# Performance work log

Measured on AMD Instinct MI355X. Metric: run time of the kernel, lower is better.

## Reference

```python
import jax, jax.numpy as jnp
import numpy as np

# dims (see shape_source): emb_dim=256, input_size=256 -> d_model=1024
B, L = 8, 1024
QUES = 4000
EMB = 256
DM = 1024          # input_size + 768
DI = 2048          # expand * d_model
N = 16             # d_state
DTR = 64           # dt_rank = ceil(d_model/16)
K = 4              # d_conv
EPS = 1e-12


def setup_inputs() -> dict:
    key = jax.random.key(0)
    ks = jax.random.split(key, 16)
    s = 0.02
    nrm = lambda k, sh: jax.random.normal(k, sh, dtype=jnp.float32) * s
    return {
        "x": jax.random.randint(ks[0], (B, L), 0, 2 * QUES + 1),
        "q_id": jax.random.randint(ks[1], (B, L), 0, QUES),
        "emb_table": nrm(ks[2], (2 * QUES + 1, EMB)),
        "ques_cont": nrm(ks[3], (QUES, 768)),
        "ln0_g": jnp.ones((DM,), jnp.float32),
        "ln0_b": jnp.zeros((DM,), jnp.float32),
        "in_proj_w": nrm(ks[4], (2 * DI, DM)),
        "conv_w": nrm(ks[5], (DI, K)),
        "conv_b": jnp.zeros((DI,), jnp.float32),
        "x_proj_w": nrm(ks[6], (DTR + 2 * N, DI)),
        "dt_proj_w": nrm(ks[7], (DI, DTR)),
        "dt_proj_b": nrm(ks[8], (DI,)),
        "A_log": jnp.log(jax.random.uniform(ks[9], (DI, N), jnp.float32, 1.0, 16.0)),
        "D_param": jnp.ones((DI,), jnp.float32),
        "out_proj_w": nrm(ks[10], (DM, DI)),
        "ln1_g": jnp.ones((DM,), jnp.float32),
        "ln1_b": jnp.zeros((DM,), jnp.float32),
        "fc_w": nrm(ks[11], (QUES, DM)),
        "fc_b": jnp.zeros((QUES,), jnp.float32),
    }


def _ln(x, g, b):
    m = x.mean(-1, keepdims=True)
    v = ((x - m) ** 2).mean(-1, keepdims=True)
    return (x - m) / jnp.sqrt(v + EPS) * g + b


def _mamba(xm, in_proj_w, conv_w, conv_b, x_proj_w, dt_proj_w, dt_proj_b,
           A_log, D_param, out_proj_w):
    # xm: [B, L, DM]
    u_r = xm @ in_proj_w.T                           # [B, L, 2*DI]
    u, r = jnp.split(u_r, 2, axis=-1)                # each [B, L, DI]
    Lq = u.shape[1]
    # causal depthwise conv1d (padding=K-1, truncated to L)
    u_pad = jnp.pad(u, ((0, 0), (K - 1, 0), (0, 0)))
    conv = sum(u_pad[:, k:k + Lq, :] * conv_w[:, k] for k in range(K)) + conv_b
    u = jax.nn.silu(conv)
    dbl = u @ x_proj_w.T                             # [B, L, DTR+2N]
    dt, Bm, Cm = dbl[..., :DTR], dbl[..., DTR:DTR + N], dbl[..., DTR + N:]
    delta = jax.nn.softplus(dt @ dt_proj_w.T + dt_proj_b)   # [B, L, DI]
    A = -jnp.exp(A_log)                              # [DI, N]

    def step(h, ins):
        d_t, b_t, c_t, u_t = ins                     # [B,DI],[B,N],[B,N],[B,DI]
        dA = jnp.exp(d_t[:, :, None] * A)            # [B, DI, N]
        h = dA * h + d_t[:, :, None] * b_t[:, None, :] * u_t[:, :, None]
        y_t = jnp.einsum('bdn,bn->bd', h, c_t)
        return h, y_t

    xs = (delta.transpose(1, 0, 2), Bm.transpose(1, 0, 2),
          Cm.transpose(1, 0, 2), u.transpose(1, 0, 2))
    h0 = jnp.zeros((u.shape[0], DI, N), u.dtype)
    _, ys = jax.lax.scan(step, h0, xs)               # ys: [L, B, DI]
    y = ys.transpose(1, 0, 2) + u * D_param
    y = y * jax.nn.silu(r)
    return y @ out_proj_w.T                          # [B, L, DM]


def reference(x, q_id, emb_table, ques_cont, ln0_g, ln0_b, in_proj_w, conv_w,
              conv_b, x_proj_w, dt_proj_w, dt_proj_b, A_log, D_param,
              out_proj_w, ln1_g, ln1_b, fc_w, fc_b):
    x_e = emb_table[x]                               # [B, L, 256]
    x_c = ques_cont[q_id]                            # [B, L, 768]
    item = _ln(jnp.concatenate([x_e, x_c], axis=-1), ln0_g, ln0_b)
    # source loop applies every layer to item_emb; only the last layer's
    # output is used, so compute exactly that one layer (num_layers=2 branch).
    h = _mamba(item, in_proj_w, conv_w, conv_b, x_proj_w, dt_proj_w,
               dt_proj_b, A_log, D_param, out_proj_w)
    out = _ln(h + item, ln1_g, ln1_b)
    return jax.nn.sigmoid(out @ fc_w.T + fc_b)       # [B, L, QUES]
```

## Files before the change

kernel.cpp:

```cpp
#include <hip/hip_runtime.h>
#include <cstdint>
#include <cstddef>

#define L_SEQ 1024
#define BATCH 8
#define DMODEL 1024
#define DINNER 2048
#define NSTATE 16
#define DTRANK 64
#define NQ 4000
#define NROWS (BATCH * L_SEQ)
#define CH 64
#define NCH (L_SEQ / CH)
#define XKN 96

typedef float f32x4 __attribute__((ext_vector_type(4)));
typedef __bf16 bf16x8 __attribute__((ext_vector_type(8)));

#define AS1 __attribute__((address_space(1)))
#define AS3 __attribute__((address_space(3)))

__device__ __forceinline__ unsigned short f2bf(float f) {
  union { float f; unsigned int u; } c; c.f = f;
  unsigned int u = c.u;
  unsigned int r = u + 0x7fffu + ((u >> 16) & 1u);
  return (unsigned short)(r >> 16);
}

__device__ __forceinline__ float sigmoidf_(float x) { return 1.f / (1.f + expf(-x)); }

__global__ void cast_bf16_k(const float* __restrict__ src, unsigned short* __restrict__ dst, int n) {
  int i = blockIdx.x * blockDim.x + threadIdx.x;
  if (i < n) dst[i] = f2bf(src[i]);
}

__device__ __forceinline__ float blk_sum(float v, float* s) {
  #pragma unroll
  for (int o = 32; o > 0; o >>= 1) v += __shfl_down(v, o, 64);
  int w = threadIdx.x >> 6;
  if ((threadIdx.x & 63) == 0) s[w] = v;
  __syncthreads();
  float r = s[0] + s[1] + s[2] + s[3];
  __syncthreads();
  return r;
}

__global__ __launch_bounds__(256) void embed_ln0_k(
    const int* __restrict__ x, const int* __restrict__ qid,
    const float* __restrict__ emb, const float* __restrict__ qc,
    const float* __restrict__ g, const float* __restrict__ bta,
    float* __restrict__ item, unsigned short* __restrict__ item_bf)
{
  __shared__ float sbuf[4];
  int i = blockIdx.x;
  int t = threadIdx.x;
  float4 v;
  if (t < 64) v = *(const float4*)&emb[(size_t)x[i] * 256 + t * 4];
  else        v = *(const float4*)&qc[(size_t)qid[i] * 768 + t * 4 - 256];
  float tot = blk_sum(v.x + v.y + v.z + v.w, sbuf);
  float mean = tot * (1.f / 1024.f);
  float dx = v.x - mean, dy = v.y - mean, dz = v.z - mean, dw = v.w - mean;
  float var = blk_sum(dx*dx + dy*dy + dz*dz + dw*dw, sbuf) * (1.f / 1024.f);
  float rstd = rsqrtf(var + 1e-12f);
  float vals[4] = {dx, dy, dz, dw};
  size_t rb = (size_t)i * 1024;
  #pragma unroll
  for (int j = 0; j < 4; j++) {
    int c = t * 4 + j;
    float o = vals[j] * rstd * g[c] + bta[c];
    item[rb + c] = o;
    item_bf[rb + c] = f2bf(o);
  }
}

template <int EPI>
__global__ __launch_bounds__(256) void gemm_bt_k(
    const unsigned short* __restrict__ A, const unsigned short* __restrict__ Bw,
    float* __restrict__ C, const float* __restrict__ bias,
    int M, int N, int K)
{
  __shared__ __align__(16) unsigned short As[128 * 64];
  __shared__ __align__(16) unsigned short Bs[128 * 64];
  const int tid = threadIdx.x;
  const int m0 = blockIdx.x * 128;
  const int n0 = blockIdx.y * 128;
  const int w = tid >> 6, lane = tid & 63;
  const int wrow = (w >> 1) * 64, wcol = (w & 1) * 64;
  const int quad = lane >> 4, lid = lane & 15;

  const int srow = lane >> 3;
  const int schunk = (lane & 7) ^ srow;

  const unsigned short* Abase = A + (size_t)(m0 + w * 8 + srow) * K + schunk * 8;
  const unsigned short* Bbase[4];
  #pragma unroll
  for (int i = 0; i < 4; i++) {
    int rB = n0 + w * 8 + i * 32 + srow;
    if (rB > N - 1) rB = N - 1;
    Bbase[i] = Bw + (size_t)rB * K + schunk * 8;
  }

  f32x4 acc[4][4] = {};

  for (int k0 = 0; k0 < K; k0 += 64) {
    #pragma unroll
    for (int i = 0; i < 4; i++) {
      int rA = w * 8 + i * 32;
      __builtin_amdgcn_global_load_lds(
          (const AS1 unsigned int*)(Abase + (size_t)i * 32 * K + k0),
          (AS3 unsigned int*)&As[rA * 64], 16, 0, 0);
      __builtin_amdgcn_global_load_lds(
          (const AS1 unsigned int*)(Bbase[i] + k0),
          (AS3 unsigned int*)&Bs[rA * 64], 16, 0, 0);
    }
    __syncthreads();
    #pragma unroll
    for (int kk = 0; kk < 64; kk += 32) {
      bf16x8 af[4], bfr[4];
      #pragma unroll
      for (int mi = 0; mi < 4; mi++) {
        int r = wrow + mi * 16 + lid;
        int slot = ((kk >> 3) + quad) ^ (lid & 7);
        af[mi] = *(const bf16x8*)&As[r * 64 + slot * 8];
      }
      #pragma unroll
      for (int ni = 0; ni < 4; ni++) {
        int r = wcol + ni * 16 + lid;
        int slot = ((kk >> 3) + quad) ^ (lid & 7);
        bfr[ni] = *(const bf16x8*)&Bs[r * 64 + slot * 8];
      }
      #pragma unroll
      for (int mi = 0; mi < 4; mi++)
        #pragma unroll
        for (int ni = 0; ni < 4; ni++)
          acc[mi][ni] = __builtin_amdgcn_mfma_f32_16x16x32_bf16(af[mi], bfr[ni], acc[mi][ni], 0, 0, 0);
    }
    __syncthreads();
  }

  #pragma unroll
  for (int mi = 0; mi < 4; mi++) {
    #pragma unroll
    for (int ni = 0; ni < 4; ni++) {
      int col = n0 + wcol + ni * 16 + lid;
      if (col >= N) continue;
      #pragma unroll
      for (int r = 0; r < 4; r++) {
        int row = m0 + wrow + mi * 16 + quad * 4 + r;
        float v = acc[mi][ni][r];
        if (EPI == 1) v = sigmoidf_(v + bias[col]);
        if (EPI == 2) { float xx = v + bias[col]; v = fmaxf(xx, 0.f) + log1pf(expf(-fabsf(xx))); }
        C[(size_t)row * N + col] = v;
      }
    }
  }
}

__global__ __launch_bounds__(256) void gemm_xk_k(
    const unsigned short* __restrict__ A, const unsigned short* __restrict__ Bw,
    float* __restrict__ slab, int M, int K, int KS)
{
  __shared__ __align__(16) unsigned short As[128 * 64];
  __shared__ __align__(16) unsigned short Bs[128 * 64];
  const int tid = threadIdx.x;
  const int m0 = blockIdx.x * 128;
  const int kslice = blockIdx.y;
  const int w = tid >> 6, lane = tid & 63;
  const int wrow = (w >> 1) * 64, wcol = (w & 1) * 64;
  const int quad = lane >> 4, lid = lane & 15;

  const int srow = lane >> 3;
  const int schunk = (lane & 7) ^ srow;

  const unsigned short* Abase = A + (size_t)(m0 + w * 8 + srow) * K + schunk * 8;
  const unsigned short* Bbase[4];
  #pragma unroll
  for (int i = 0; i < 4; i++) {
    int rB = w * 8 + i * 32 + srow;
    if (rB > XKN - 1) rB = XKN - 1;
    Bbase[i] = Bw + (size_t)rB * K + schunk * 8;
  }

  f32x4 acc[4][4] = {};
  const int kbeg = kslice * KS, kend = kbeg + KS;

  for (int k0 = kbeg; k0 < kend; k0 += 64) {
    #pragma unroll
    for (int i = 0; i < 4; i++) {
      int rA = w * 8 + i * 32;
      __builtin_amdgcn_global_load_lds(
          (const AS1 unsigned int*)(Abase + (size_t)i * 32 * K + k0),
          (AS3 unsigned int*)&As[rA * 64], 16, 0, 0);
      __builtin_amdgcn_global_load_lds(
          (const AS1 unsigned int*)(Bbase[i] + k0),
          (AS3 unsigned int*)&Bs[rA * 64], 16, 0, 0);
    }
    __syncthreads();
    #pragma unroll
    for (int kk = 0; kk < 64; kk += 32) {
      bf16x8 af[4], bfr[4];
      #pragma unroll
      for (int mi = 0; mi < 4; mi++) {
        int r = wrow + mi * 16 + lid;
        int slot = ((kk >> 3) + quad) ^ (lid & 7);
        af[mi] = *(const bf16x8*)&As[r * 64 + slot * 8];
      }
      #pragma unroll
      for (int ni = 0; ni < 4; ni++) {
        int r = wcol + ni * 16 + lid;
        int slot = ((kk >> 3) + quad) ^ (lid & 7);
        bfr[ni] = *(const bf16x8*)&Bs[r * 64 + slot * 8];
      }
      #pragma unroll
      for (int mi = 0; mi < 4; mi++)
        #pragma unroll
        for (int ni = 0; ni < 4; ni++)
          acc[mi][ni] = __builtin_amdgcn_mfma_f32_16x16x32_bf16(af[mi], bfr[ni], acc[mi][ni], 0, 0, 0);
    }
    __syncthreads();
  }

  float* Cs = slab + (size_t)kslice * M * XKN;
  #pragma unroll
  for (int mi = 0; mi < 4; mi++) {
    #pragma unroll
    for (int ni = 0; ni < 4; ni++) {
      int col = wcol + ni * 16 + lid;
      if (col >= XKN) continue;
      #pragma unroll
      for (int r = 0; r < 4; r++) {
        int row = m0 + wrow + mi * 16 + quad * 4 + r;
        Cs[(size_t)row * XKN + col] = acc[mi][ni][r];
      }
    }
  }
}

__global__ void xproj_reduce_k(const float* __restrict__ slab, float* __restrict__ dbl,
                               unsigned short* __restrict__ dt_bf)
{
  int i = blockIdx.x * blockDim.x + threadIdx.x;
  if (i >= NROWS * XKN) return;
  const size_t S = (size_t)NROWS * XKN;
  float s = slab[i] + slab[i + S] + slab[i + 2 * S] + slab[i + 3 * S];
  dbl[i] = s;
  int row = i / XKN, col = i - row * XKN;
  if (col < 64) dt_bf[(size_t)row * 64 + col] = f2bf(s);
}

__global__ void conv_silu_k(const float* __restrict__ u_r, const float* __restrict__ w,
                            const float* __restrict__ cb, float* __restrict__ uc,
                            unsigned short* __restrict__ uc_bf)
{
  int idx = blockIdx.x * blockDim.x + threadIdx.x;
  if (idx >= BATCH * L_SEQ * DINNER) return;
  int d = idx & (DINNER - 1);
  int l = (idx >> 11) & (L_SEQ - 1);
  int b = idx >> 21;
  float4 wv = ((const float4*)w)[d];
  size_t rb = ((size_t)b * L_SEQ + l) * (2 * DINNER) + d;
  float acc = cb[d];
  acc += wv.w * u_r[rb];
  if (l >= 1) acc += wv.z * u_r[rb - (2 * DINNER)];
  if (l >= 2) acc += wv.y * u_r[rb - 2 * (2 * DINNER)];
  if (l >= 3) acc += wv.x * u_r[rb - 3 * (2 * DINNER)];
  float s = acc * sigmoidf_(acc);
  uc[idx] = s;
  uc_bf[idx] = f2bf(s);
}

__global__ void a2_k(const float* __restrict__ Alog, float* __restrict__ a2t)
{
  int i = blockIdx.x * blockDim.x + threadIdx.x;
  if (i >= DINNER * NSTATE) return;
  int d = i >> 4, n = i & 15;
  a2t[n * DINNER + d] = -expf(Alog[i]) * 1.4426950408889634f;
}

__global__ __launch_bounds__(64) void scan1_k(
    const float* __restrict__ dlt, const float* __restrict__ uc,
    const float* __restrict__ dbl, const float* __restrict__ a2t,
    float* __restrict__ Pbuf, float* __restrict__ Qbuf)
{
  int c = blockIdx.x;
  int dg = blockIdx.y;
  int b = blockIdx.z;
  int d = dg * 64 + threadIdx.x;
  float a2[NSTATE], P[NSTATE], q[NSTATE];
  #pragma unroll
  for (int n = 0; n < NSTATE; n++) {
    a2[n] = a2t[n * DINNER + d];
    P[n] = 1.f; q[n] = 0.f;
  }
  size_t base = ((size_t)(b * L_SEQ + c * CH)) * DINNER + d;
  const float* bc = dbl + (size_t)(b * L_SEQ + c * CH) * XKN + 64;
  for (int t = 0; t < CH; t++) {
    float dl = dlt[base];
    float du = dl * uc[base];
    #pragma unroll
    for (int n = 0; n < NSTATE; n++) {
      float dA = exp2f(dl * a2[n]);
      q[n] = dA * q[n] + du * bc[n];
      P[n] *= dA;
    }
    base += DINNER;
    bc += XKN;
  }
  size_t ob = ((size_t)((b * NCH + c) * NSTATE)) * DINNER + d;
  #pragma unroll
  for (int n = 0; n < NSTATE; n++) {
    Pbuf[ob + (size_t)n * DINNER] = P[n];
    Qbuf[ob + (size_t)n * DINNER] = q[n];
  }
}

__global__ void scan_carry_k(const float* __restrict__ Pbuf, float* __restrict__ Qbuf)
{
  int idx = blockIdx.x * blockDim.x + threadIdx.x;
  if (idx >= BATCH * NSTATE * DINNER) return;
  int d = idx & (DINNER - 1);
  int n = (idx >> 11) & 15;
  int b = idx >> 15;
  float h = 0.f;
  for (int c = 0; c < NCH; c++) {
    size_t o = ((size_t)((b * NCH + c) * NSTATE + n)) * DINNER + d;
    float P = Pbuf[o];
    float q = Qbuf[o];
    Qbuf[o] = h;
    h = P * h + q;
  }
}

__global__ __launch_bounds__(64) void scan2_k(
    const float* __restrict__ dlt, const float* __restrict__ uc,
    const float* __restrict__ dbl, const float* __restrict__ a2t,
    const float* __restrict__ Qbuf, const float* __restrict__ u_r,
    const float* __restrict__ Dp, unsigned short* __restrict__ ybf)
{
  int c = blockIdx.x;
  int dg = blockIdx.y;
  int b = blockIdx.z;
  int d = dg * 64 + threadIdx.x;
  float a2[NSTATE], h[NSTATE];
  size_t ob = ((size_t)((b * NCH + c) * NSTATE)) * DINNER + d;
  #pragma unroll
  for (int n = 0; n < NSTATE; n++) {
    a2[n] = a2t[n * DINNER + d];
    h[n] = Qbuf[ob + (size_t)n * DINNER];
  }
  float Dd = Dp[d];
  size_t base = ((size_t)(b * L_SEQ + c * CH)) * DINNER + d;
  const float* bc = dbl + (size_t)(b * L_SEQ + c * CH) * XKN + 64;
  const float* rp = u_r + (size_t)(b * L_SEQ + c * CH) * (2 * DINNER) + DINNER + d;
  for (int t = 0; t < CH; t++) {
    float dl = dlt[base];
    float uval = uc[base];
    float du = dl * uval;
    float yv = 0.f;
    #pragma unroll
    for (int n = 0; n < NSTATE; n++) {
      float dA = exp2f(dl * a2[n]);
      h[n] = dA * h[n] + du * bc[n];
      yv += h[n] * bc[NSTATE + n];
    }
    float rv = *rp;
    float val = (yv + uval * Dd) * (rv * sigmoidf_(rv));
    ybf[base] = f2bf(val);
    base += DINNER;
    bc += XKN;
    rp += 2 * DINNER;
  }
}

__global__ __launch_bounds__(256) void ln1_k(
    const float* __restrict__ mamba, const float* __restrict__ item,
    const float* __restrict__ g, const float* __restrict__ bta,
    unsigned short* __restrict__ out_bf)
{
  __shared__ float sbuf[4];
  int i = blockIdx.x;
  int t = threadIdx.x;
  size_t rb = (size_t)i * 1024 + t * 4;
  float4 v = *(const float4*)&mamba[rb];
  float4 w4 = *(const float4*)&item[rb];
  v.x += w4.x; v.y += w4.y; v.z += w4.z; v.w += w4.w;
  float tot = blk_sum(v.x + v.y + v.z + v.w, sbuf);
  float mean = tot * (1.f / 1024.f);
  float dx = v.x - mean, dy = v.y - mean, dz = v.z - mean, dw = v.w - mean;
  float var = blk_sum(dx*dx + dy*dy + dz*dz + dw*dw, sbuf) * (1.f / 1024.f);
  float rstd = rsqrtf(var + 1e-12f);
  float vals[4] = {dx, dy, dz, dw};
  #pragma unroll
  for (int j = 0; j < 4; j++) {
    int c = t * 4 + j;
    out_bf[(size_t)i * 1024 + c] = f2bf(vals[j] * rstd * g[c] + bta[c]);
  }
}

extern "C" void kernel_launch(void* const* d_in, const int* in_sizes, int n_in,
                              void* d_out, int out_size, void* d_ws, size_t ws_size,
                              hipStream_t stream)
{
  (void)in_sizes; (void)n_in; (void)out_size; (void)ws_size;
  const int*   x     = (const int*)d_in[0];
  const int*   qid   = (const int*)d_in[1];
  const float* emb   = (const float*)d_in[2];
  const float* qc    = (const float*)d_in[3];
  const float* ln0g  = (const float*)d_in[4];
  const float* ln0b  = (const float*)d_in[5];
  const float* w_in  = (const float*)d_in[6];
  const float* convw = (const float*)d_in[7];
  const float* convb = (const float*)d_in[8];
  const float* w_x   = (const float*)d_in[9];
  const float* w_dt  = (const float*)d_in[10];
  const float* dtb   = (const float*)d_in[11];
  const float* Alog  = (const float*)d_in[12];
  const float* Dp    = (const float*)d_in[13];
  const float* w_out = (const float*)d_in[14];
  const float* ln1g  = (const float*)d_in[15];
  const float* ln1b  = (const float*)d_in[16];
  const float* w_fc  = (const float*)d_in[17];
  const float* fcb   = (const float*)d_in[18];
  float* out = (float*)d_out;

  char* base = (char*)d_ws;
  size_t off = 0;
  auto carve = [&](size_t bytes) -> char* {
    char* p = base + off;
    off = (off + bytes + 255) & ~(size_t)255;
    return p;
  };
  float* item  = (float*)carve((size_t)NROWS * 1024 * 4);
  float* u_r   = (float*)carve((size_t)NROWS * 4096 * 4);
  float* uc    = (float*)carve((size_t)NROWS * 2048 * 4);
  float* dbl   = (float*)carve((size_t)NROWS * XKN * 4);
  float* dlt   = (float*)carve((size_t)NROWS * 2048 * 4);
  float* mamba = (float*)carve((size_t)NROWS * 1024 * 4);
  unsigned short* bfbuf  = (unsigned short*)carve((size_t)NROWS * 2048 * 2);
  unsigned short* bw_in  = (unsigned short*)carve((size_t)4096 * 1024 * 2);
  unsigned short* bw_x   = (unsigned short*)carve((size_t)XKN * 2048 * 2);
  unsigned short* bw_dt  = (unsigned short*)carve((size_t)2048 * 64 * 2);
  unsigned short* bw_out = (unsigned short*)carve((size_t)1024 * 2048 * 2);
  unsigned short* bw_fc  = (unsigned short*)carve((size_t)4000 * 1024 * 2);
  float* a2t   = (float*)carve((size_t)DINNER * NSTATE * 4);

  float* slab = dlt;
  unsigned short* dt_bf = (unsigned short*)mamba;
  float* Pbuf = mamba;
  float* Qbuf = (float*)bfbuf;
  unsigned short* y_bf = (unsigned short*)mamba;
  float* mamba_out = u_r;

  auto cv = [&](const float* s, unsigned short* dst, int n) {
    cast_bf16_k<<<(n + 255) / 256, 256, 0, stream>>>(s, dst, n);
  };
  cv(w_in,  bw_in,  4096 * 1024);
  cv(w_x,   bw_x,   XKN * 2048);
  cv(w_dt,  bw_dt,  2048 * 64);
  cv(w_out, bw_out, 1024 * 2048);
  cv(w_fc,  bw_fc,  4000 * 1024);
  a2_k<<<(DINNER * NSTATE + 255) / 256, 256, 0, stream>>>(Alog, a2t);

  embed_ln0_k<<<NROWS, 256, 0, stream>>>(x, qid, emb, qc, ln0g, ln0b, item, bfbuf);

  gemm_bt_k<0><<<dim3(64, 32), 256, 0, stream>>>(bfbuf, bw_in, u_r, nullptr, NROWS, 4096, 1024);

  conv_silu_k<<<(NROWS * DINNER) / 256, 256, 0, stream>>>(u_r, convw, convb, uc, bfbuf);

  gemm_xk_k<<<dim3(64, 4), 256, 0, stream>>>(bfbuf, bw_x, slab, NROWS, 2048, 512);
  xproj_reduce_k<<<(NROWS * XKN) / 256, 256, 0, stream>>>(slab, dbl, dt_bf);

  gemm_bt_k<2><<<dim3(64, 16), 256, 0, stream>>>(dt_bf, bw_dt, dlt, dtb, NROWS, 2048, 64);

  scan1_k<<<dim3(NCH, 32, BATCH), 64, 0, stream>>>(dlt, uc, dbl, a2t, Pbuf, Qbuf);
  scan_carry_k<<<(BATCH * NSTATE * DINNER) / 256, 256, 0, stream>>>(Pbuf, Qbuf);
  scan2_k<<<dim3(NCH, 32, BATCH), 64, 0, stream>>>(dlt, uc, dbl, a2t, Qbuf, u_r, Dp, y_bf);

  gemm_bt_k<0><<<dim3(64, 8), 256, 0, stream>>>(y_bf, bw_out, mamba_out, nullptr, NROWS, 1024, 2048);

  ln1_k<<<NROWS, 256, 0, stream>>>(mamba_out, item, ln1g, ln1b, bfbuf);

  gemm_bt_k<1><<<dim3(64, 32), 256, 0, stream>>>(bfbuf, bw_fc, out, fcb, NROWS, 4000, 1024);
}
```

Measured before the change: 855.3 us.

## Store intermediate activations in bf16 and vectorize conv_silu

Intermediates that were written as fp32 are now stored as bf16: the in_proj output, the conv/SiLU output, the out_proj output and the LayerNorm0 item buffer. A new GEMM epilogue mode writes bf16, and conv_silu now handles four channels per thread with ushort4 loads and stores. This roughly halves the memory traffic of the conv, scan and LN1 stages, but adds bf16 rounding to the residual path, the gate r and the scan input u, which lowers accuracy. Note that the main GEMM's bf16 stores are 2-byte scalar writes scattered across columns.

```diff
diff --git a/kernel.cpp b/kernel.cpp
--- a/kernel.cpp
+++ b/kernel.cpp
@@ -27,6 +27,11 @@
   return (unsigned short)(r >> 16);
 }
 
+__device__ __forceinline__ float bf2f(unsigned short h) {
+  union { unsigned int u; float f; } c; c.u = (unsigned int)h << 16;
+  return c.f;
+}
+
 __device__ __forceinline__ float sigmoidf_(float x) { return 1.f / (1.f + expf(-x)); }
 
 __global__ void cast_bf16_k(const float* __restrict__ src, unsigned short* __restrict__ dst, int n) {
@@ -49,7 +54,7 @@
     const int* __restrict__ x, const int* __restrict__ qid,
     const float* __restrict__ emb, const float* __restrict__ qc,
     const float* __restrict__ g, const float* __restrict__ bta,
-    float* __restrict__ item, unsigned short* __restrict__ item_bf)
+    unsigned short* __restrict__ item_bf)
 {
   __shared__ float sbuf[4];
   int i = blockIdx.x;
@@ -67,9 +72,7 @@
   #pragma unroll
   for (int j = 0; j < 4; j++) {
     int c = t * 4 + j;
-    float o = vals[j] * rstd * g[c] + bta[c];
-    item[rb + c] = o;
-    item_bf[rb + c] = f2bf(o);
+    item_bf[rb + c] = f2bf(vals[j] * rstd * g[c] + bta[c]);
   }
 }
 
@@ -150,7 +153,8 @@
         float v = acc[mi][ni][r];
         if (EPI == 1) v = sigmoidf_(v + bias[col]);
         if (EPI == 2) { float xx = v + bias[col]; v = fmaxf(xx, 0.f) + log1pf(expf(-fabsf(xx))); }
-        C[(size_t)row * N + col] = v;
+        if (EPI == 4) ((unsigned short*)C)[(size_t)row * N + col] = f2bf(v);
+        else          C[(size_t)row * N + col] = v;
       }
     }
   }
@@ -248,25 +252,47 @@
   if (col < 64) dt_bf[(size_t)row * 64 + col] = f2bf(s);
 }
 
-__global__ void conv_silu_k(const float* __restrict__ u_r, const float* __restrict__ w,
-                            const float* __restrict__ cb, float* __restrict__ uc,
-                            unsigned short* __restrict__ uc_bf)
+__global__ void conv_silu_k(const unsigned short* __restrict__ u_r, const float* __restrict__ w,
+                            const float* __restrict__ cb, unsigned short* __restrict__ uc_bf)
 {
   int idx = blockIdx.x * blockDim.x + threadIdx.x;
-  if (idx >= BATCH * L_SEQ * DINNER) return;
-  int d = idx & (DINNER - 1);
-  int l = (idx >> 11) & (L_SEQ - 1);
-  int b = idx >> 21;
-  float4 wv = ((const float4*)w)[d];
+  if (idx >= BATCH * L_SEQ * DINNER / 4) return;
+  int dd = idx & (DINNER / 4 - 1);
+  int l = (idx >> 9) & (L_SEQ - 1);
+  int b = idx >> 19;
+  int d = dd * 4;
+  float4 wv[4];
+  #pragma unroll
+  for (int j = 0; j < 4; j++) wv[j] = ((const float4*)w)[d + j];
+  float4 cbv = *(const float4*)&cb[d];
+  float acc[4] = {cbv.x, cbv.y, cbv.z, cbv.w};
   size_t rb = ((size_t)b * L_SEQ + l) * (2 * DINNER) + d;
-  float acc = cb[d];
-  acc += wv.w * u_r[rb];
-  if (l >= 1) acc += wv.z * u_r[rb - (2 * DINNER)];
-  if (l >= 2) acc += wv.y * u_r[rb - 2 * (2 * DINNER)];
-  if (l >= 3) acc += wv.x * u_r[rb - 3 * (2 * DINNER)];
-  float s = acc * sigmoidf_(acc);
-  uc[idx] = s;
-  uc_bf[idx] = f2bf(s);
+  {
+    ushort4 uv = *(const ushort4*)&u_r[rb];
+    acc[0] += wv[0].w * bf2f(uv.x); acc[1] += wv[1].w * bf2f(uv.y);
+    acc[2] += wv[2].w * bf2f(uv.z); acc[3] += wv[3].w * bf2f(uv.w);
+  }
+  if (l >= 1) {
+    ushort4 uv = *(const ushort4*)&u_r[rb - (size_t)(2 * DINNER)];
+    acc[0] += wv[0].z * bf2f(uv.x); acc[1] += wv[1].z * bf2f(uv.y);
+    acc[2] += wv[2].z * bf2f(uv.z); acc[3] += wv[3].z * bf2f(uv.w);
+  }
+  if (l >= 2) {
+    ushort4 uv = *(const ushort4*)&u_r[rb - (size_t)2 * (2 * DINNER)];
+    acc[0] += wv[0].y * bf2f(uv.x); acc[1] += wv[1].y * bf2f(uv.y);
+    acc[2] += wv[2].y * bf2f(uv.z); acc[3] += wv[3].y * bf2f(uv.w);
+  }
+  if (l >= 3) {
+    ushort4 uv = *(const ushort4*)&u_r[rb - (size_t)3 * (2 * DINNER)];
+    acc[0] += wv[0].x * bf2f(uv.x); acc[1] += wv[1].x * bf2f(uv.y);
+    acc[2] += wv[2].x * bf2f(uv.z); acc[3] += wv[3].x * bf2f(uv.w);
+  }
+  ushort4 o;
+  o.x = f2bf(acc[0] * sigmoidf_(acc[0]));
+  o.y = f2bf(acc[1] * sigmoidf_(acc[1]));
+  o.z = f2bf(acc[2] * sigmoidf_(acc[2]));
+  o.w = f2bf(acc[3] * sigmoidf_(acc[3]));
+  *(ushort4*)&uc_bf[((size_t)(b * L_SEQ + l)) * DINNER + d] = o;
 }
 
 __global__ void a2_k(const float* __restrict__ Alog, float* __restrict__ a2t)
@@ -278,7 +304,7 @@
 }
 
 __global__ __launch_bounds__(64) void scan1_k(
-    const float* __restrict__ dlt, const float* __restrict__ uc,
+    const float* __restrict__ dlt, const unsigned short* __restrict__ uc,
     const float* __restrict__ dbl, const float* __restrict__ a2t,
     float* __restrict__ Pbuf, float* __restrict__ Qbuf)
 {
@@ -296,7 +322,7 @@
   const float* bc = dbl + (size_t)(b * L_SEQ + c * CH) * XKN + 64;
   for (int t = 0; t < CH; t++) {
     float dl = dlt[base];
-    float du = dl * uc[base];
+    float du = dl * bf2f(uc[base]);
     #pragma unroll
     for (int n = 0; n < NSTATE; n++) {
       float dA = exp2f(dl * a2[n]);
@@ -332,9 +358,9 @@
 }
 
 __global__ __launch_bounds__(64) void scan2_k(
-    const float* __restrict__ dlt, const float* __restrict__ uc,
+    const float* __restrict__ dlt, const unsigned short* __restrict__ uc,
     const float* __restrict__ dbl, const float* __restrict__ a2t,
-    const float* __restrict__ Qbuf, const float* __restrict__ u_r,
+    const float* __restrict__ Qbuf, const unsigned short* __restrict__ u_r,
     const float* __restrict__ Dp, unsigned short* __restrict__ ybf)
 {
   int c = blockIdx.x;
@@ -351,10 +377,10 @@
   float Dd = Dp[d];
   size_t base = ((size_t)(b * L_SEQ + c * CH)) * DINNER + d;
   const float* bc = dbl + (size_t)(b * L_SEQ + c * CH) * XKN + 64;
-  const float* rp = u_r + (size_t)(b * L_SEQ + c * CH) * (2 * DINNER) + DINNER + d;
+  const unsigned short* rp = u_r + (size_t)(b * L_SEQ + c * CH) * (2 * DINNER) + DINNER + d;
   for (int t = 0; t < CH; t++) {
     float dl = dlt[base];
-    float uval = uc[base];
+    float uval = bf2f(uc[base]);
     float du = dl * uval;
     float yv = 0.f;
     #pragma unroll
@@ -363,7 +389,7 @@
       h[n] = dA * h[n] + du * bc[n];
       yv += h[n] * bc[NSTATE + n];
     }
-    float rv = *rp;
+    float rv = bf2f(*rp);
     float val = (yv + uval * Dd) * (rv * sigmoidf_(rv));
     ybf[base] = f2bf(val);
     base += DINNER;
@@ -373,7 +399,7 @@
 }
 
 __global__ __launch_bounds__(256) void ln1_k(
-    const float* __restrict__ mamba, const float* __restrict__ item,
+    const unsigned short* __restrict__ mamba, const unsigned short* __restrict__ item,
     const float* __restrict__ g, const float* __restrict__ bta,
     unsigned short* __restrict__ out_bf)
 {
@@ -381,12 +407,15 @@
   int i = blockIdx.x;
   int t = threadIdx.x;
   size_t rb = (size_t)i * 1024 + t * 4;
-  float4 v = *(const float4*)&mamba[rb];
-  float4 w4 = *(const float4*)&item[rb];
-  v.x += w4.x; v.y += w4.y; v.z += w4.z; v.w += w4.w;
-  float tot = blk_sum(v.x + v.y + v.z + v.w, sbuf);
+  ushort4 mv = *(const ushort4*)&mamba[rb];
+  ushort4 iv = *(const ushort4*)&item[rb];
+  float vx = bf2f(mv.x) + bf2f(iv.x);
+  float vy = bf2f(mv.y) + bf2f(iv.y);
+  float vz = bf2f(mv.z) + bf2f(iv.z);
+  float vw = bf2f(mv.w) + bf2f(iv.w);
+  float tot = blk_sum(vx + vy + vz + vw, sbuf);
   float mean = tot * (1.f / 1024.f);
-  float dx = v.x - mean, dy = v.y - mean, dz = v.z - mean, dw = v.w - mean;
+  float dx = vx - mean, dy = vy - mean, dz = vz - mean, dw = vw - mean;
   float var = blk_sum(dx*dx + dy*dy + dz*dz + dw*dw, sbuf) * (1.f / 1024.f);
   float rstd = rsqrtf(var + 1e-12f);
   float vals[4] = {dx, dy, dz, dw};
@@ -430,9 +459,9 @@
     off = (off + bytes + 255) & ~(size_t)255;
     return p;
   };
-  float* item  = (float*)carve((size_t)NROWS * 1024 * 4);
-  float* u_r   = (float*)carve((size_t)NROWS * 4096 * 4);
-  float* uc    = (float*)carve((size_t)NROWS * 2048 * 4);
+  unsigned short* item_bf = (unsigned short*)carve((size_t)NROWS * 1024 * 2);
+  unsigned short* u_r     = (unsigned short*)carve((size_t)NROWS * 4096 * 2);
+  unsigned short* ucbf    = (unsigned short*)carve((size_t)NROWS * 2048 * 2);
   float* dbl   = (float*)carve((size_t)NROWS * XKN * 4);
   float* dlt   = (float*)carve((size_t)NROWS * 2048 * 4);
   float* mamba = (float*)carve((size_t)NROWS * 1024 * 4);
@@ -449,7 +478,7 @@
   float* Pbuf = mamba;
   float* Qbuf = (float*)bfbuf;
   unsigned short* y_bf = (unsigned short*)mamba;
-  float* mamba_out = u_r;
+  unsigned short* mamba_out = u_r;
 
   auto cv = [&](const float* s, unsigned short* dst, int n) {
     cast_bf16_k<<<(n + 255) / 256, 256, 0, stream>>>(s, dst, n);
@@ -461,24 +490,24 @@
   cv(w_fc,  bw_fc,  4000 * 1024);
   a2_k<<<(DINNER * NSTATE + 255) / 256, 256, 0, stream>>>(Alog, a2t);
 
-  embed_ln0_k<<<NROWS, 256, 0, stream>>>(x, qid, emb, qc, ln0g, ln0b, item, bfbuf);
-
-  gemm_bt_k<0><<<dim3(64, 32), 256, 0, stream>>>(bfbuf, bw_in, u_r, nullptr, NROWS, 4096, 1024);
-
-  conv_silu_k<<<(NROWS * DINNER) / 256, 256, 0, stream>>>(u_r, convw, convb, uc, bfbuf);
-
-  gemm_xk_k<<<dim3(64, 4), 256, 0, stream>>>(bfbuf, bw_x, slab, NROWS, 2048, 512);
+  embed_ln0_k<<<NROWS, 256, 0, stream>>>(x, qid, emb, qc, ln0g, ln0b, item_bf);
+
+  gemm_bt_k<4><<<dim3(64, 32), 256, 0, stream>>>(item_bf, bw_in, (float*)u_r, nullptr, NROWS, 4096, 1024);
+
+  conv_silu_k<<<(NROWS * DINNER / 4) / 256, 256, 0, stream>>>(u_r, convw, convb, ucbf);
+
+  gemm_xk_k<<<dim3(64, 4), 256, 0, stream>>>(ucbf, bw_x, slab, NROWS, 2048, 512);
   xproj_reduce_k<<<(NROWS * XKN) / 256, 256, 0, stream>>>(slab, dbl, dt_bf);
 
   gemm_bt_k<2><<<dim3(64, 16), 256, 0, stream>>>(dt_bf, bw_dt, dlt, dtb, NROWS, 2048, 64);
 
-  scan1_k<<<dim3(NCH, 32, BATCH), 64, 0, stream>>>(dlt, uc, dbl, a2t, Pbuf, Qbuf);
+  scan1_k<<<dim3(NCH, 32, BATCH), 64, 0, stream>>>(dlt, ucbf, dbl, a2t, Pbuf, Qbuf);
   scan_carry_k<<<(BATCH * NSTATE * DINNER) / 256, 256, 0, stream>>>(Pbuf, Qbuf);
-  scan2_k<<<dim3(NCH, 32, BATCH), 64, 0, stream>>>(dlt, uc, dbl, a2t, Qbuf, u_r, Dp, y_bf);
-
-  gemm_bt_k<0><<<dim3(64, 8), 256, 0, stream>>>(y_bf, bw_out, mamba_out, nullptr, NROWS, 1024, 2048);
-
-  ln1_k<<<NROWS, 256, 0, stream>>>(mamba_out, item, ln1g, ln1b, bfbuf);
+  scan2_k<<<dim3(NCH, 32, BATCH), 64, 0, stream>>>(dlt, ucbf, dbl, a2t, Qbuf, u_r, Dp, y_bf);
+
+  gemm_bt_k<4><<<dim3(64, 8), 256, 0, stream>>>(y_bf, bw_out, (float*)mamba_out, nullptr, NROWS, 1024, 2048);
+
+  ln1_k<<<NROWS, 256, 0, stream>>>(mamba_out, item_bf, ln1g, ln1b, bfbuf);
 
   gemm_bt_k<1><<<dim3(64, 32), 256, 0, stream>>>(bfbuf, bw_fc, out, fcb, NROWS, 4000, 1024);
 }
```

Result: faster. 822.7 us (-3.8%).
